# Optimization experiments

Measured on AMD Instinct MI355X. Metric: run time of the kernel, lower is better.

The kernel has to match this reference:

```python
import jax, jax.numpy as jnp
import numpy as np

B, T, H = 4, 4096, 1024


def setup_inputs() -> dict:
    key = jax.random.key(0)
    k1, k2 = jax.random.split(key)
    h = jax.random.normal(k1, (B, T, H), dtype=jnp.float32)
    # nn.Linear weight, scaled for stable magnitudes
    W = jax.random.normal(k2, (H, H), dtype=jnp.float32) / np.sqrt(H).astype(np.float32)
    return {"h": h, "W": W, "T_hist": 256}


def reference(h, W, T_hist):
    Bb, Tt, Hh = h.shape
    # K = Linear(h) = h @ W.T ; Q = V = h
    K = jnp.einsum('bth,oh->bto', h, W)
    scores = jnp.einsum('bqh,bkh->bqk', h, K) / jnp.sqrt(jnp.asarray(Hh, h.dtype))
    # banded mask: causal (j <= i) AND limited history (j >= i - (T_hist-1))
    i = jnp.arange(Tt)[:, None]
    j = jnp.arange(Tt)[None, :]
    valid = (j <= i) & (j >= i - (T_hist - 1))
    scores = jnp.where(valid[None, :, :], scores, -jnp.inf)
    attn = jax.nn.softmax(scores, axis=-1)
    attn = jnp.nan_to_num(attn, nan=0.0)  # matches torch nan_to_num(0.0)
    context = jnp.einsum('bqk,bkh->bqh', attn, h)
    return context
```

## Files before the change

kernel.cpp:

```cpp
#include <hip/hip_runtime.h>
#include <hip/hip_bf16.h>

#define B_ 4
#define T_ 4096
#define H_ 1024
#define WP2 320

typedef short  s16x8 __attribute__((ext_vector_type(8)));
typedef float  f32x4 __attribute__((ext_vector_type(4)));
typedef unsigned short u16;

static __device__ __forceinline__ u16 bf16rn(float f) {
  unsigned int u = __float_as_uint(f);
  u += 0x7fffu + ((u >> 16) & 1u);
  return (u16)(u >> 16);
}

static __device__ __forceinline__ void gl2lds16(const u16* g, u16* l) {
  __builtin_amdgcn_global_load_lds(
      (__attribute__((address_space(1))) void*)(g),
      (__attribute__((address_space(3))) void*)(l), 16, 0, 0);
}

__global__ __launch_bounds__(256) void k_convT(const float* __restrict__ h,
                                               u16* __restrict__ hb,
                                               u16* __restrict__ hbT) {
  __shared__ unsigned int tile32[64 * 33];
  const int b  = blockIdx.z;
  const int t0 = blockIdx.y * 64;
  const int c0 = blockIdx.x * 64;
  const int t  = threadIdx.x;
  {
    const int r  = t >> 2;
    const int cq = (t & 3) << 4;
    const size_t g = (size_t)(b * T_ + t0 + r) * H_ + c0 + cq;
    const f32x4* src = (const f32x4*)(h + g);
    u16 o[16];
#pragma unroll
    for (int v = 0; v < 4; ++v) {
      f32x4 x = src[v];
#pragma unroll
      for (int j = 0; j < 4; ++j) o[v * 4 + j] = bf16rn(x[j]);
    }
    s16x8 w0, w1;
#pragma unroll
    for (int j = 0; j < 8; ++j) { w0[j] = (short)o[j]; w1[j] = (short)o[8 + j]; }
    *(s16x8*)(hb + g)     = w0;
    *(s16x8*)(hb + g + 8) = w1;
#pragma unroll
    for (int i = 0; i < 8; ++i)
      tile32[r * 33 + (cq >> 1) + i] =
          (unsigned int)o[2 * i] | ((unsigned int)o[2 * i + 1] << 16);
  }
  __syncthreads();
  {
    const int fpair = t & 31;
    const int kq    = t >> 5;
    unsigned int v[8];
#pragma unroll
    for (int j = 0; j < 8; ++j) v[j] = tile32[(kq * 8 + j) * 33 + fpair];
    s16x8 w0, w1;
#pragma unroll
    for (int j = 0; j < 8; ++j) {
      w0[j] = (short)(v[j] & 0xffffu);
      w1[j] = (short)(v[j] >> 16);
    }
    const size_t o0 = (size_t)(b * H_ + c0 + 2 * fpair) * T_ + t0 + kq * 8;
    *(s16x8*)(hbT + o0)      = w0;
    *(s16x8*)(hbT + o0 + T_) = w1;
  }
}

__global__ __launch_bounds__(256) void k_convW(const float* __restrict__ src,
                                               u16* __restrict__ dst) {
  const int i = (blockIdx.x * 256 + threadIdx.x) * 8;
  f32x4 a = *(const f32x4*)(src + i);
  f32x4 b = *(const f32x4*)(src + i + 4);
  s16x8 w;
#pragma unroll
  for (int j = 0; j < 4; ++j) {
    w[j]     = (short)bf16rn(a[j]);
    w[4 + j] = (short)bf16rn(b[j]);
  }
  *(s16x8*)(dst + i) = w;
}

__global__ __launch_bounds__(256) void k_gemmK(const u16* __restrict__ hb,
                                               const u16* __restrict__ Wb,
                                               u16* __restrict__ Kb) {
  __shared__ __align__(16) u16 As[3][512 * 8];
  __shared__ __align__(16) u16 Bs[3][512 * 8];
  const int t = threadIdx.x;
  const int id  = blockIdx.y * gridDim.x + blockIdx.x;
  const int swz = (id & 7) * 128 + (id >> 3);
  const int row0 = (swz >> 3) * 128;
  const int col0 = (swz & 7) * 128;
  const int lane = t & 63, wv = t >> 6;
  const int wr = wv >> 1, wc = wv & 1;
  const int l15 = lane & 15, quad = lane >> 4;

  const int c0 = t, c1 = t + 256;
  const size_t gA0 = (size_t)(row0 + (c0 >> 2)) * H_ + (c0 & 3) * 8;
  const size_t gA1 = (size_t)(row0 + (c1 >> 2)) * H_ + (c1 & 3) * 8;
  const size_t gB0 = (size_t)(col0 + (c0 >> 2)) * H_ + (c0 & 3) * 8;
  const size_t gB1 = (size_t)(col0 + (c1 >> 2)) * H_ + (c1 & 3) * 8;

  f32x4 acc[4][4];
#pragma unroll
  for (int m = 0; m < 4; ++m)
#pragma unroll
    for (int n = 0; n < 4; ++n) acc[m][n] = (f32x4)0.0f;

  gl2lds16(hb + gA0, &As[0][c0 * 8]);
  gl2lds16(hb + gA1, &As[0][c1 * 8]);
  gl2lds16(Wb + gB0, &Bs[0][c0 * 8]);
  gl2lds16(Wb + gB1, &Bs[0][c1 * 8]);
  gl2lds16(hb + gA0 + 32, &As[1][c0 * 8]);
  gl2lds16(hb + gA1 + 32, &As[1][c1 * 8]);
  gl2lds16(Wb + gB0 + 32, &Bs[1][c0 * 8]);
  gl2lds16(Wb + gB1 + 32, &Bs[1][c1 * 8]);
  asm volatile("s_waitcnt vmcnt(4)" ::: "memory");
  __builtin_amdgcn_s_barrier();

#pragma unroll
  for (int kt = 0; kt < 32; ++kt) {
    if (kt + 2 < 32) {
      const int sn = (kt + 2) % 3;
      const int off = (kt + 2) * 32;
      gl2lds16(hb + gA0 + off, &As[sn][c0 * 8]);
      gl2lds16(hb + gA1 + off, &As[sn][c1 * 8]);
      gl2lds16(Wb + gB0 + off, &Bs[sn][c0 * 8]);
      gl2lds16(Wb + gB1 + off, &Bs[sn][c1 * 8]);
    }
    const int sc = kt % 3;
    s16x8 aF[4], bF[4];
#pragma unroll
    for (int mt = 0; mt < 4; ++mt)
      aF[mt] = *(const s16x8*)&As[sc][((wr * 64 + mt * 16 + l15) * 4 + quad) * 8];
#pragma unroll
    for (int nt = 0; nt < 4; ++nt)
      bF[nt] = *(const s16x8*)&Bs[sc][((wc * 64 + nt * 16 + l15) * 4 + quad) * 8];
#pragma unroll
    for (int mt = 0; mt < 4; ++mt)
#pragma unroll
      for (int nt = 0; nt < 4; ++nt)
        acc[mt][nt] = __builtin_amdgcn_mfma_f32_16x16x32_bf16(aF[mt], bF[nt],
                                                              acc[mt][nt], 0, 0, 0);
    if (kt + 1 < 32) {
      if (kt <= 29) asm volatile("s_waitcnt vmcnt(4)" ::: "memory");
      else          asm volatile("s_waitcnt vmcnt(0)" ::: "memory");
      __builtin_amdgcn_s_barrier();
    }
  }
#pragma unroll
  for (int mt = 0; mt < 4; ++mt)
#pragma unroll
    for (int nt = 0; nt < 4; ++nt)
#pragma unroll
      for (int r = 0; r < 4; ++r) {
        const int row = row0 + wr * 64 + mt * 16 + quad * 4 + r;
        const int col = col0 + wc * 64 + nt * 16 + l15;
        Kb[(size_t)row * H_ + col] = bf16rn(acc[mt][nt][r]);
      }
}

__global__ __launch_bounds__(512) void k_scores(const u16* __restrict__ hb,
                                                const u16* __restrict__ Kb,
                                                u16* __restrict__ P) {
  __shared__ __align__(16) u16 Ks[2][1152 * 8];
  __shared__ float Sred[2][4][16];
  const int t = threadIdx.x;
  const int wv = t >> 6, lane = t & 63;
  const int l15 = lane & 15, quad = lane >> 4;
  const int id  = blockIdx.x;
  const int swz = (id & 7) * 64 + (id >> 3);
  const int b  = swz >> 7;
  const int q0 = (swz & 127) * 32;
  const int qt = wv & 1;
  const int sub = wv >> 1;
  const int qt0 = q0 + qt * 16;
  const int ktbase = (sub == 0) ? 0 : (1 + sub * 4);
  const int nkt = (sub == 0) ? 5 : 4;

  const u16* qbase = hb + (size_t)(b * T_ + qt0 + l15) * H_ + quad * 8;

  const u16* kst[3];
  int cid[3];
#pragma unroll
  for (int p = 0; p < 3; ++p) {
    int c = p * 512 + t;
    if (c > 1151) c = 1151;
    cid[p] = c;
    const int m = c >> 6, lr = (c >> 2) & 15, qd = c & 3;
    int tok = q0 - 256 + m * 16 + lr;
    if (tok < 0) tok = 0;
    kst[p] = Kb + (size_t)(b * T_ + tok) * H_ + qd * 8;
  }
  const bool p2 = (t < 128);

  f32x4 acc[5];
#pragma unroll
  for (int i = 0; i < 5; ++i) acc[i] = (f32x4)0.0f;

  gl2lds16(kst[0], &Ks[0][cid[0] * 8]);
  gl2lds16(kst[1], &Ks[0][cid[1] * 8]);
  if (p2) gl2lds16(kst[2], &Ks[0][cid[2] * 8]);
  __syncthreads();

  int cur = 0;
  for (int s = 0; s < 32; ++s) {
    if (s + 1 < 32) {
      const int off = (s + 1) * 32;
      gl2lds16(kst[0] + off, &Ks[cur ^ 1][cid[0] * 8]);
      gl2lds16(kst[1] + off, &Ks[cur ^ 1][cid[1] * 8]);
      if (p2) gl2lds16(kst[2] + off, &Ks[cur ^ 1][cid[2] * 8]);
    }
    const s16x8 aQ = *(const s16x8*)(qbase + s * 32);
#pragma unroll
    for (int i = 0; i < 5; ++i) {
      if (i < nkt) {
        const int m = qt + ktbase + i;
        const s16x8 bK = *(const s16x8*)&Ks[cur][(m * 64 + l15 * 4 + quad) * 8];
        acc[i] = __builtin_amdgcn_mfma_f32_16x16x32_bf16(aQ, bK, acc[i], 0, 0, 0);
      }
    }
    __syncthreads();
    cur ^= 1;
  }

  const float scale = 0.03125f;
#pragma unroll
  for (int r = 0; r < 4; ++r) {
    const int q = qt0 + quad * 4 + r;
    float sum = 0.0f;
#pragma unroll
    for (int i = 0; i < 5; ++i) {
      if (i < nkt) {
        const int k = qt0 - 256 + (ktbase + i) * 16 + l15;
        const bool valid = (k >= 0) && (k <= q) && (k >= q - 255);
        const float p = valid ? __expf(acc[i][r] * scale) : 0.0f;
        acc[i][r] = p;
        sum += p;
      }
    }
    sum += __shfl_xor(sum, 1);
    sum += __shfl_xor(sum, 2);
    sum += __shfl_xor(sum, 4);
    sum += __shfl_xor(sum, 8);
    if (l15 == 0) Sred[qt][sub][quad * 4 + r] = sum;
  }
  __syncthreads();
  const int toff = ((q0 & 32) >> 4) + qt;
#pragma unroll
  for (int r = 0; r < 4; ++r) {
    const int q = qt0 + quad * 4 + r;
    const int row = quad * 4 + r;
    const float inv = 1.0f / (Sred[qt][0][row] + Sred[qt][1][row] +
                              Sred[qt][2][row] + Sred[qt][3][row]);
    u16* prow = P + (size_t)(b * T_ + q) * WP2;
#pragma unroll
    for (int i = 0; i < 5; ++i)
      if (i < nkt) prow[(toff + ktbase + i) * 16 + l15] = bf16rn(acc[i][r] * inv);
    if (sub == 0) {
#pragma unroll
      for (int z = 0; z < 3; ++z) {
        const int slot = (toff + 17 + z) % 20;
        prow[slot * 16 + l15] = 0;
      }
    }
  }
}

__global__ __launch_bounds__(512) void k_ctx(const u16* __restrict__ P,
                                             const u16* __restrict__ hbT,
                                             float* __restrict__ out) {
  __shared__ __align__(16) u16 Vs[2][1280 * 8];
  const int t = threadIdx.x;
  const int wv = t >> 6, lane = t & 63;
  const int l15 = lane & 15, quad = lane >> 4;
  const int id  = blockIdx.x;
  const int swz = (id & 7) * 64 + (id >> 3);
  const int fhalf = swz & 1;
  const int blk   = swz >> 1;
  const int b  = blk >> 6;
  const int q0 = (blk & 63) * 64;
  const int qtile = wv & 3, fh = wv >> 2;
  const int qt0 = q0 + qtile * 16;

  const u16* prow = P + (size_t)(b * T_ + qt0 + l15) * WP2 + quad * 8;
  s16x8 aP[10];
#pragma unroll
  for (int c = 0; c < 10; ++c) aP[c] = *(const s16x8*)(prow + c * 32);

  const int tok0 = q0 - 256;
  const u16* vst[3];
  int cid[3];
#pragma unroll
  for (int p = 0; p < 3; ++p) {
    int c = p * 512 + t;
    if (c > 1279) c = 1279;
    cid[p] = c;
    const int cg = c >> 7, ft = (c >> 6) & 1, lr = (c >> 2) & 15, qd = c & 3;
    const int fr = ft * 16 + lr;
    int tok = tok0 + (cg * 4 + qd) * 8;
    if (tok < 0) tok = 0;
    vst[p] = hbT + (size_t)(b * H_ + fr) * T_ + tok;
  }
  const bool p2 = (t < 256);
  const size_t fbase = (size_t)(fhalf * 512) * T_;
  const size_t fstep = (size_t)32 * T_;

  gl2lds16(vst[0] + fbase, &Vs[0][cid[0] * 8]);
  gl2lds16(vst[1] + fbase, &Vs[0][cid[1] * 8]);
  if (p2) gl2lds16(vst[2] + fbase, &Vs[0][cid[2] * 8]);
  __syncthreads();

  int cur = 0;
  for (int g = 0; g < 16; ++g) {
    if (g + 1 < 16) {
      const size_t off = fbase + (size_t)(g + 1) * fstep;
      gl2lds16(vst[0] + off, &Vs[cur ^ 1][cid[0] * 8]);
      gl2lds16(vst[1] + off, &Vs[cur ^ 1][cid[1] * 8]);
      if (p2) gl2lds16(vst[2] + off, &Vs[cur ^ 1][cid[2] * 8]);
    }
    f32x4 acc = (f32x4)0.0f;
#pragma unroll
    for (int c = 0; c < 10; ++c) {
      const s16x8 bv =
          *(const s16x8*)&Vs[cur][(c * 128 + fh * 64 + l15 * 4 + quad) * 8];
      acc = __builtin_amdgcn_mfma_f32_16x16x32_bf16(aP[c], bv, acc, 0, 0, 0);
    }
    __syncthreads();
    const int f0 = (fhalf * 16 + g) * 32 + fh * 16 + l15;
#pragma unroll
    for (int r = 0; r < 4; ++r)
      out[(size_t)(b * T_ + qt0 + quad * 4 + r) * H_ + f0] = acc[r];
    cur ^= 1;
  }
}

extern "C" void kernel_launch(void* const* d_in, const int* in_sizes, int n_in,
                              void* d_out, int out_size, void* d_ws, size_t ws_size,
                              hipStream_t stream) {
  const float* h  = (const float*)d_in[0];
  const float* Wf = (const float*)d_in[1];

  char* ws = (char*)d_ws;
  u16* hb  = (u16*)(ws);
  u16* hbT = (u16*)(ws + (size_t)33554432);
  u16* Kb  = (u16*)(ws + (size_t)67108864);
  u16* Wb  = (u16*)(ws + (size_t)100663296);
  u16* P   = (u16*)(ws + (size_t)102760448);
  float* out = (float*)d_out;

  k_convT <<<dim3(H_ / 64, T_ / 64, B_), 256, 0, stream>>>(h, hb, hbT);
  k_convW <<<dim3(512), 256, 0, stream>>>(Wf, Wb);
  k_gemmK <<<dim3(H_ / 128, (B_ * T_) / 128), 256, 0, stream>>>(hb, Wb, Kb);
  k_scores<<<dim3((B_ * T_) / 32), 512, 0, stream>>>(hb, Kb, P);
  k_ctx   <<<dim3(2 * (B_ * T_) / 64), 512, 0, stream>>>(P, hbT, out);
}
```

Baseline: 227.1 us.

## Triple-buffer LDS prefetch two stages ahead and stage Q tiles through LDS

Both the scores and the context kernels move from a double-buffered LDS ring to a three-slot ring, issuing global-to-LDS loads two steps ahead. Full __syncthreads waits are replaced by partial s_waitcnt vmcnt waits plus a raw barrier, so newer loads stay in flight while the current tile is consumed. In the scores kernel, the Q fragment is also loaded into LDS alongside K instead of being read directly from global memory every step. The aim is to hide global load latency behind MFMA work, at the cost of more LDS per block (possibly lower occupancy). The hand-counted vmcnt values are fragile, including the store accounting in the context kernel.

```diff
diff --git a/kernel.cpp b/kernel.cpp
--- a/kernel.cpp
+++ b/kernel.cpp
@@ -167,7 +167,7 @@
 __global__ __launch_bounds__(512) void k_scores(const u16* __restrict__ hb,
                                                 const u16* __restrict__ Kb,
                                                 u16* __restrict__ P) {
-  __shared__ __align__(16) u16 Ks[2][1152 * 8];
+  __shared__ __align__(16) u16 Ks[3][1280 * 8];
   __shared__ float Sred[2][4][16];
   const int t = threadIdx.x;
   const int wv = t >> 6, lane = t & 63;
@@ -182,50 +182,69 @@
   const int ktbase = (sub == 0) ? 0 : (1 + sub * 4);
   const int nkt = (sub == 0) ? 5 : 4;
 
-  const u16* qbase = hb + (size_t)(b * T_ + qt0 + l15) * H_ + quad * 8;
-
-  const u16* kst[3];
+  const u16* st[3];
   int cid[3];
 #pragma unroll
   for (int p = 0; p < 3; ++p) {
     int c = p * 512 + t;
-    if (c > 1151) c = 1151;
+    if (c > 1279) c = 1279;
     cid[p] = c;
-    const int m = c >> 6, lr = (c >> 2) & 15, qd = c & 3;
-    int tok = q0 - 256 + m * 16 + lr;
-    if (tok < 0) tok = 0;
-    kst[p] = Kb + (size_t)(b * T_ + tok) * H_ + qd * 8;
-  }
-  const bool p2 = (t < 128);
+    if (c < 1152) {
+      const int m = c >> 6, lr = (c >> 2) & 15, qd = c & 3;
+      int tok = q0 - 256 + m * 16 + lr;
+      if (tok < 0) tok = 0;
+      st[p] = Kb + (size_t)(b * T_ + tok) * H_ + qd * 8;
+    } else {
+      const int qc = c - 1152;
+      const int r = qc >> 2, qd = qc & 3;
+      st[p] = hb + (size_t)(b * T_ + q0 + r) * H_ + qd * 8;
+    }
+  }
+  const bool w03 = (t < 256);
 
   f32x4 acc[5];
 #pragma unroll
   for (int i = 0; i < 5; ++i) acc[i] = (f32x4)0.0f;
 
-  gl2lds16(kst[0], &Ks[0][cid[0] * 8]);
-  gl2lds16(kst[1], &Ks[0][cid[1] * 8]);
-  if (p2) gl2lds16(kst[2], &Ks[0][cid[2] * 8]);
-  __syncthreads();
-
-  int cur = 0;
+  gl2lds16(st[0], &Ks[0][cid[0] * 8]);
+  gl2lds16(st[1], &Ks[0][cid[1] * 8]);
+  if (w03) gl2lds16(st[2], &Ks[0][cid[2] * 8]);
+  gl2lds16(st[0] + 32, &Ks[1][cid[0] * 8]);
+  gl2lds16(st[1] + 32, &Ks[1][cid[1] * 8]);
+  if (w03) gl2lds16(st[2] + 32, &Ks[1][cid[2] * 8]);
+  if (w03) asm volatile("s_waitcnt vmcnt(3)" ::: "memory");
+  else     asm volatile("s_waitcnt vmcnt(2)" ::: "memory");
+  __builtin_amdgcn_s_barrier();
+
+#pragma unroll
   for (int s = 0; s < 32; ++s) {
-    if (s + 1 < 32) {
-      const int off = (s + 1) * 32;
-      gl2lds16(kst[0] + off, &Ks[cur ^ 1][cid[0] * 8]);
-      gl2lds16(kst[1] + off, &Ks[cur ^ 1][cid[1] * 8]);
-      if (p2) gl2lds16(kst[2] + off, &Ks[cur ^ 1][cid[2] * 8]);
-    }
-    const s16x8 aQ = *(const s16x8*)(qbase + s * 32);
+    if (s + 2 < 32) {
+      const int sn = (s + 2) % 3;
+      const int off = (s + 2) * 32;
+      gl2lds16(st[0] + off, &Ks[sn][cid[0] * 8]);
+      gl2lds16(st[1] + off, &Ks[sn][cid[1] * 8]);
+      if (w03) gl2lds16(st[2] + off, &Ks[sn][cid[2] * 8]);
+    }
+    const int sc = s % 3;
+    const s16x8 aQ =
+        *(const s16x8*)&Ks[sc][(1152 + (qt * 16 + l15) * 4 + quad) * 8];
 #pragma unroll
     for (int i = 0; i < 5; ++i) {
       if (i < nkt) {
         const int m = qt + ktbase + i;
-        const s16x8 bK = *(const s16x8*)&Ks[cur][(m * 64 + l15 * 4 + quad) * 8];
+        const s16x8 bK = *(const s16x8*)&Ks[sc][(m * 64 + l15 * 4 + quad) * 8];
         acc[i] = __builtin_amdgcn_mfma_f32_16x16x32_bf16(aQ, bK, acc[i], 0, 0, 0);
       }
     }
-    __syncthreads();
-    cur ^= 1;
+    if (s + 1 < 32) {
+      if (s <= 29) {
+        if (w03) asm volatile("s_waitcnt vmcnt(3)" ::: "memory");
+        else     asm volatile("s_waitcnt vmcnt(2)" ::: "memory");
+      } else {
+        asm volatile("s_waitcnt vmcnt(0)" ::: "memory");
+      }
+      __builtin_amdgcn_s_barrier();
+    }
   }
 
   const float scale = 0.03125f;
@@ -274,7 +293,7 @@
 __global__ __launch_bounds__(512) void k_ctx(const u16* __restrict__ P,
                                              const u16* __restrict__ hbT,
                                              float* __restrict__ out) {
-  __shared__ __align__(16) u16 Vs[2][1280 * 8];
+  __shared__ __align__(16) u16 Vs[3][1280 * 8];
   const int t = threadIdx.x;
   const int wv = t >> 6, lane = t & 63;
   const int l15 = lane & 15, quad = lane >> 4;
@@ -306,36 +325,50 @@
     if (tok < 0) tok = 0;
     vst[p] = hbT + (size_t)(b * H_ + fr) * T_ + tok;
   }
-  const bool p2 = (t < 256);
+  const bool w03 = (t < 256);
   const size_t fbase = (size_t)(fhalf * 512) * T_;
   const size_t fstep = (size_t)32 * T_;
 
   gl2lds16(vst[0] + fbase, &Vs[0][cid[0] * 8]);
   gl2lds16(vst[1] + fbase, &Vs[0][cid[1] * 8]);
-  if (p2) gl2lds16(vst[2] + fbase, &Vs[0][cid[2] * 8]);
-  __syncthreads();
-
-  int cur = 0;
+  if (w03) gl2lds16(vst[2] + fbase, &Vs[0][cid[2] * 8]);
+  gl2lds16(vst[0] + fbase + fstep, &Vs[1][cid[0] * 8]);
+  gl2lds16(vst[1] + fbase + fstep, &Vs[1][cid[1] * 8]);
+  if (w03) gl2lds16(vst[2] + fbase + fstep, &Vs[1][cid[2] * 8]);
+  if (w03) asm volatile("s_waitcnt vmcnt(3)" ::: "memory");
+  else     asm volatile("s_waitcnt vmcnt(2)" ::: "memory");
+  __builtin_amdgcn_s_barrier();
+
+#pragma unroll
   for (int g = 0; g < 16; ++g) {
-    if (g + 1 < 16) {
-      const size_t off = fbase + (size_t)(g + 1) * fstep;
-      gl2lds16(vst[0] + off, &Vs[cur ^ 1][cid[0] * 8]);
-      gl2lds16(vst[1] + off, &Vs[cur ^ 1][cid[1] * 8]);
-      if (p2) gl2lds16(vst[2] + off, &Vs[cur ^ 1][cid[2] * 8]);
-    }
+    if (g + 2 < 16) {
+      const int sn = (g + 2) % 3;
+      const size_t off = fbase + (size_t)(g + 2) * fstep;
+      gl2lds16(vst[0] + off, &Vs[sn][cid[0] * 8]);
+      gl2lds16(vst[1] + off, &Vs[sn][cid[1] * 8]);
+      if (w03) gl2lds16(vst[2] + off, &Vs[sn][cid[2] * 8]);
+    }
+    const int sc = g % 3;
     f32x4 acc = (f32x4)0.0f;
 #pragma unroll
     for (int c = 0; c < 10; ++c) {
       const s16x8 bv =
-          *(const s16x8*)&Vs[cur][(c * 128 + fh * 64 + l15 * 4 + quad) * 8];
+          *(const s16x8*)&Vs[sc][(c * 128 + fh * 64 + l15 * 4 + quad) * 8];
       acc = __builtin_amdgcn_mfma_f32_16x16x32_bf16(aP[c], bv, acc, 0, 0, 0);
     }
-    __syncthreads();
+    if (g + 1 < 16) {
+      if (g <= 13) {
+        if (w03) asm volatile("s_waitcnt vmcnt(7)" ::: "memory");
+        else     asm volatile("s_waitcnt vmcnt(6)" ::: "memory");
+      } else {
+        asm volatile("s_waitcnt vmcnt(4)" ::: "memory");
+      }
+      __builtin_amdgcn_s_barrier();
+    }
     const int f0 = (fhalf * 16 + g) * 32 + fh * 16 + l15;
 #pragma unroll
     for (int r = 0; r < 4; ++r)
       out[(size_t)(b * T_ + qt0 + quad * 4 + r) * H_ + f0] = acc[r];
-    cur ^= 1;
   }
 }
 
```

Measured after the change: 221.4 us. -2.5%, faster.
